# Optimization experiments

Measured on AMD Instinct MI355X. Metric: run time of the kernel, lower is better.

Reference implementation:

```python
import jax, jax.numpy as jnp
import numpy as np

B, C, L = 4, 256, 4096
H = 8
DK = C // H


def setup_inputs() -> dict:
    key = jax.random.key(0)
    kx, kq, kk, kv, kl = jax.random.split(key, 5)
    scale = 1.0 / np.sqrt(C)
    return {
        "x": jax.random.normal(kx, (B, C, L), dtype=jnp.float32),
        "Wq": jax.random.normal(kq, (C, C), dtype=jnp.float32) * scale,
        "Wk": jax.random.normal(kk, (C, C), dtype=jnp.float32) * scale,
        "Wv": jax.random.normal(kv, (C, C), dtype=jnp.float32) * scale,
        "Wl": jax.random.normal(kl, (C, C), dtype=jnp.float32) * scale,
    }


def reference(x, Wq, Wk, Wv, Wl):
    # Conv1d with kernel_size=1, no bias == channel-mixing matmul per position.
    def proj(W, t):  # W: [C_out, C_in], t: [B, C_in, L] -> [B, L, H, DK]
        y = jnp.einsum('oc,bcl->blo', W, t)
        return y.reshape(B, L, H, DK)

    q = proj(Wq, x)  # [B, L, H, DK]
    k = proj(Wk, x)
    v = proj(Wv, x)

    # scores: [B, H, L, L]
    scores = jnp.einsum('bqhd,bkhd->bhqk', q, k) / jnp.sqrt(jnp.float32(DK))
    p_attn = jax.nn.softmax(scores, axis=-1)
    # attention output with post-ReLU: [B, L, H, DK] -> [B, L, C]
    out = jax.nn.relu(jnp.einsum('bhqk,bkhd->bqhd', p_attn, v)).reshape(B, L, C)
    # last_conv: [B, C_out, L]
    return jnp.einsum('oc,blc->bol', Wl, out)
```

## Files before the change

kernel.cpp:

```cpp
#include <hip/hip_runtime.h>

#define L_DIM 4096
#define C_DIM 256
#define B_DIM 4
#define NH 8
#define DK 32

#define QSCALE 0.25507694f

typedef __bf16 bf16x8 __attribute__((ext_vector_type(8)));
typedef float  f32x4  __attribute__((ext_vector_type(4)));
typedef float  f32x16 __attribute__((ext_vector_type(16)));

static __device__ __forceinline__ unsigned pk_bf16(float lo, float hi) {
    unsigned a = __builtin_bit_cast(unsigned, lo) + 0x8000u;
    unsigned b = __builtin_bit_cast(unsigned, hi) + 0x8000u;
    return __builtin_amdgcn_perm(b, a, 0x07060302u);
}

__global__ __launch_bounds__(256) void transpose_x_kernel(
    const float* __restrict__ x, __bf16* __restrict__ xt)
{
    const int t  = threadIdx.x;
    const int l0 = blockIdx.x * 64;
    const int c0 = blockIdx.y * 64;
    const int b  = blockIdx.z;

    __shared__ __attribute__((aligned(16))) float T[64][65];

    {
        const int r  = t >> 2;
        const int lc = (t & 3) * 16;
        const float* xp = x + ((size_t)b * C_DIM + c0 + r) * L_DIM + l0 + lc;
        #pragma unroll
        for (int k = 0; k < 4; ++k)
            *(f32x4*)&T[r][lc + k * 4] = *(const f32x4*)(xp + k * 4);
    }
    __syncthreads();
    {
        const int l  = t >> 2;
        const int cc = (t & 3) * 16;
        unsigned u[8];
        #pragma unroll
        for (int i = 0; i < 8; ++i)
            u[i] = pk_bf16(T[cc + 2 * i][l], T[cc + 2 * i + 1][l]);
        __bf16* op = xt + ((size_t)b * L_DIM + l0 + l) * C_DIM + c0 + cc;
        *(uint4*)op       = make_uint4(u[0], u[1], u[2], u[3]);
        *(uint4*)(op + 8) = make_uint4(u[4], u[5], u[6], u[7]);
    }
}

__global__ __launch_bounds__(256) void proj_mfma_kernel(
    const __bf16* __restrict__ xt, const float* __restrict__ Wq,
    const float* __restrict__ Wk, const float* __restrict__ Wv,
    __bf16* __restrict__ Qb, __bf16* __restrict__ Kb, __bf16* __restrict__ Vb)
{
    const int t    = threadIdx.x;
    const int wave = t >> 6;
    const int lane = t & 63;
    const int n32  = lane & 31;
    const int hl   = lane >> 5;
    const int l0   = blockIdx.x * 128;
    const int ob   = blockIdx.y & 1;
    const int p    = blockIdx.y >> 1;
    const int b    = blockIdx.z;
    const float* W = (p == 0) ? Wq : ((p == 1) ? Wk : Wv);
    const float sc = (p == 0) ? QSCALE : 1.0f;

    __shared__ __attribute__((aligned(16))) __bf16 Wt[128][72];
    __shared__ __attribute__((aligned(16))) __bf16 Xs[128][72];

    const int wo  = t >> 1, wcc = (t & 1) * 32;
    const int xl  = t >> 1, xcc = (t & 1) * 32;
    const float*  wg = W + (size_t)(ob * 128 + wo) * C_DIM + wcc;
    const __bf16* xg = xt + ((size_t)b * L_DIM + l0 + xl) * C_DIM + xcc;

    const int moff = (wave & 1) * 64;
    const int noff = (wave >> 1) * 64;

    f32x16 acc[2][2];
    #pragma unroll
    for (int i = 0; i < 2; ++i)
        #pragma unroll
        for (int j = 0; j < 2; ++j)
            #pragma unroll
            for (int r = 0; r < 16; ++r) acc[i][j][r] = 0.f;

    unsigned wpk[16];
    bf16x8   xpr[4];
    #pragma unroll
    for (int k = 0; k < 8; ++k) {
        f32x4 wv = *(const f32x4*)(wg + k * 4);
        wpk[k * 2]     = pk_bf16(wv[0] * sc, wv[1] * sc);
        wpk[k * 2 + 1] = pk_bf16(wv[2] * sc, wv[3] * sc);
    }
    #pragma unroll
    for (int g = 0; g < 4; ++g) xpr[g] = *(const bf16x8*)(xg + g * 8);

    for (int bk = 0; bk < 4; ++bk) {
        __syncthreads();
        #pragma unroll
        for (int g = 0; g < 4; ++g) {
            *(uint4*)&Wt[wo][wcc + g * 8] =
                make_uint4(wpk[g*4], wpk[g*4+1], wpk[g*4+2], wpk[g*4+3]);
            *(bf16x8*)&Xs[xl][xcc + g * 8] = xpr[g];
        }
        if (bk < 3) {
            #pragma unroll
            for (int k = 0; k < 8; ++k) {
                f32x4 wv = *(const f32x4*)(wg + (bk + 1) * 64 + k * 4);
                wpk[k * 2]     = pk_bf16(wv[0] * sc, wv[1] * sc);
                wpk[k * 2 + 1] = pk_bf16(wv[2] * sc, wv[3] * sc);
            }
            #pragma unroll
            for (int g = 0; g < 4; ++g)
                xpr[g] = *(const bf16x8*)(xg + (bk + 1) * 64 + g * 8);
        }
        __syncthreads();

        #pragma unroll
        for (int ks = 0; ks < 4; ++ks) {
            bf16x8 a0 = *(const bf16x8*)&Wt[moff + n32     ][ks * 16 + hl * 8];
            bf16x8 a1 = *(const bf16x8*)&Wt[moff + 32 + n32][ks * 16 + hl * 8];
            bf16x8 b0 = *(const bf16x8*)&Xs[noff + n32     ][ks * 16 + hl * 8];
            bf16x8 b1 = *(const bf16x8*)&Xs[noff + 32 + n32][ks * 16 + hl * 8];
            acc[0][0] = __builtin_amdgcn_mfma_f32_32x32x16_bf16(a0, b0, acc[0][0], 0, 0, 0);
            acc[0][1] = __builtin_amdgcn_mfma_f32_32x32x16_bf16(a0, b1, acc[0][1], 0, 0, 0);
            acc[1][0] = __builtin_amdgcn_mfma_f32_32x32x16_bf16(a1, b0, acc[1][0], 0, 0, 0);
            acc[1][1] = __builtin_amdgcn_mfma_f32_32x32x16_bf16(a1, b1, acc[1][1], 0, 0, 0);
        }
    }

    #pragma unroll
    for (int mt = 0; mt < 2; ++mt) {
        const int o32 = ob * 128 + moff + mt * 32;
        const int h   = o32 >> 5;
        const int bh  = b * NH + h;
        #pragma unroll
        for (int nt = 0; nt < 2; ++nt) {
            const int l = l0 + noff + nt * 32 + n32;
            if (p < 2) {
                __bf16* out = ((p == 0) ? Qb : Kb) + ((size_t)bh * L_DIM + l) * DK;
                #pragma unroll
                for (int g = 0; g < 4; ++g) {
                    unsigned u0 = pk_bf16(acc[mt][nt][g*4],     acc[mt][nt][g*4+1]);
                    unsigned u1 = pk_bf16(acc[mt][nt][g*4+2],   acc[mt][nt][g*4+3]);
                    *(uint2*)(out + 4 * hl + 8 * g) = make_uint2(u0, u1);
                }
            } else {
                #pragma unroll
                for (int r = 0; r < 16; ++r) {
                    const int dk = (r & 3) + 4 * hl + 8 * (r >> 2);
                    Vb[((size_t)bh * DK + dk) * L_DIM + l] = (__bf16)acc[mt][nt][r];
                }
            }
        }
    }
}

__global__ __launch_bounds__(256) void attn_kernel(
    const __bf16* __restrict__ Q, const __bf16* __restrict__ K,
    const __bf16* __restrict__ V, __bf16* __restrict__ Op0,
    __bf16* __restrict__ Op1, float* __restrict__ Ls)
{
    const int tid   = threadIdx.x;
    const int wave  = tid >> 6;
    const int lane  = tid & 63;
    const int n32   = lane & 31;
    const int hl    = lane >> 5;
    const int h     = blockIdx.y;
    const int b     = blockIdx.z >> 1;
    const int khalf = blockIdx.z & 1;
    const int bh    = b * NH + h;
    const int q0    = blockIdx.x * 256 + wave * 64;
    const int kt0   = khalf * 32;

    __shared__ __attribute__((aligned(16))) __bf16 Ks[64][40];
    __shared__ __attribute__((aligned(16))) __bf16 Vs[32][72];

    bf16x8 qf[2][2];
    #pragma unroll
    for (int qt = 0; qt < 2; ++qt) {
        const __bf16* qp = Q + ((size_t)bh * L_DIM + q0 + qt * 32 + n32) * DK;
        qf[qt][0] = *(const bf16x8*)(qp + hl * 8);
        qf[qt][1] = *(const bf16x8*)(qp + 16 + hl * 8);
    }

    f32x16 oacc[2], lacc[2];
    #pragma unroll
    for (int qt = 0; qt < 2; ++qt)
        #pragma unroll
        for (int r = 0; r < 16; ++r) { oacc[qt][r] = 0.f; lacc[qt][r] = 0.f; }

    const f32x16 z16 = {};

    bf16x8 ones;
    #pragma unroll
    for (int j = 0; j < 8; ++j) ones[j] = (__bf16)1.0f;

    const __bf16* kg = K + (size_t)bh * L_DIM * DK + (tid >> 2) * DK + (tid & 3) * 8;
    const __bf16* vg = V + ((size_t)bh * DK + (tid >> 3)) * L_DIM + (tid & 7) * 8;
    __bf16* ksd = &Ks[tid >> 2][(tid & 3) * 8];
    const int va  = tid & 7;
    __bf16* vsd0 = &Vs[tid >> 3][(va >> 1) * 16 + (va & 1) * 4];
    __bf16* vsd1 = vsd0 + 8;

    bf16x8 kreg = *(const bf16x8*)(kg + (size_t)kt0 * 64 * DK);
    bf16x8 vreg = *(const bf16x8*)(vg + kt0 * 64);

    for (int kt = 0; kt < 32; ++kt) {
        __syncthreads();
        *(bf16x8*)ksd = kreg;
        union { bf16x8 v; uint2 u2[2]; } vv; vv.v = vreg;
        *(uint2*)vsd0 = vv.u2[0];
        *(uint2*)vsd1 = vv.u2[1];
        {
            const int nkt = kt0 + ((kt + 1) & 31);
            kreg = *(const bf16x8*)(kg + (size_t)nkt * 64 * DK);
            vreg = *(const bf16x8*)(vg + nkt * 64);
        }
        __syncthreads();

        bf16x8 kf[2][2];
        kf[0][0] = *(const bf16x8*)&Ks[n32     ][hl * 8];
        kf[0][1] = *(const bf16x8*)&Ks[n32     ][16 + hl * 8];
        kf[1][0] = *(const bf16x8*)&Ks[32 + n32][hl * 8];
        kf[1][1] = *(const bf16x8*)&Ks[32 + n32][16 + hl * 8];
        bf16x8 vf[4];
        vf[0] = *(const bf16x8*)&Vs[n32][     hl * 8];
        vf[1] = *(const bf16x8*)&Vs[n32][16 + hl * 8];
        vf[2] = *(const bf16x8*)&Vs[n32][32 + hl * 8];
        vf[3] = *(const bf16x8*)&Vs[n32][48 + hl * 8];

        #pragma unroll
        for (int mt = 0; mt < 2; ++mt) {
            #pragma unroll
            for (int qt = 0; qt < 2; ++qt) {
                f32x16 s = __builtin_amdgcn_mfma_f32_32x32x16_bf16(
                    kf[mt][0], qf[qt][0], z16, 0, 0, 0);
                s = __builtin_amdgcn_mfma_f32_32x32x16_bf16(
                    kf[mt][1], qf[qt][1], s, 0, 0, 0);

                float e[16];
                #pragma unroll
                for (int r = 0; r < 16; ++r) e[r] = __builtin_amdgcn_exp2f(s[r]);
                union { unsigned u[4]; bf16x8 v; } p0, p1;
                #pragma unroll
                for (int i = 0; i < 4; ++i) {
                    p0.u[i] = pk_bf16(e[2 * i],     e[2 * i + 1]);
                    p1.u[i] = pk_bf16(e[8 + 2 * i], e[8 + 2 * i + 1]);
                }

                oacc[qt] = __builtin_amdgcn_mfma_f32_32x32x16_bf16(
                    vf[mt * 2],     p0.v, oacc[qt], 0, 0, 0);
                lacc[qt] = __builtin_amdgcn_mfma_f32_32x32x16_bf16(
                    ones,           p0.v, lacc[qt], 0, 0, 0);
                oacc[qt] = __builtin_amdgcn_mfma_f32_32x32x16_bf16(
                    vf[mt * 2 + 1], p1.v, oacc[qt], 0, 0, 0);
                lacc[qt] = __builtin_amdgcn_mfma_f32_32x32x16_bf16(
                    ones,           p1.v, lacc[qt], 0, 0, 0);
            }
        }
    }

    __bf16* Op = khalf ? Op1 : Op0;
    #pragma unroll
    for (int qt = 0; qt < 2; ++qt) {
        const int l = q0 + qt * 32 + n32;
        __bf16* ap = Op + ((size_t)b * L_DIM + l) * C_DIM + h * 32 + 4 * hl;
        #pragma unroll
        for (int g = 0; g < 4; ++g) {
            *(uint2*)(ap + 8 * g) = make_uint2(
                pk_bf16(oacc[qt][g*4],     oacc[qt][g*4+1]),
                pk_bf16(oacc[qt][g*4+2],   oacc[qt][g*4+3]));
        }
        Ls[((size_t)khalf * B_DIM * NH + bh) * L_DIM + l] = lacc[qt][0];
    }
}

__global__ __launch_bounds__(256) void final_mfma_kernel(
    const __bf16* __restrict__ Op0, const __bf16* __restrict__ Op1,
    const float* __restrict__ Ls, const float* __restrict__ Wl,
    float* __restrict__ y)
{
    const int t    = threadIdx.x;
    const int wave = t >> 6;
    const int lane = t & 63;
    const int n32  = lane & 31;
    const int hl   = lane >> 5;
    const int l0   = blockIdx.x * 64;
    const int ob   = blockIdx.y;
    const int b    = blockIdx.z;

    __shared__ __attribute__((aligned(16))) __bf16 Wt[128][72];
    __shared__ __attribute__((aligned(16))) __bf16 Xs[64][72];

    const int wo  = t >> 1, wcc = (t & 1) * 32;
    const int xl  = t >> 2, xcc = (t & 3) * 16;
    const float* wg = Wl + (size_t)(ob * 128 + wo) * C_DIM + wcc;
    const size_t obase = ((size_t)b * L_DIM + l0 + xl) * C_DIM + xcc;

    float inv[4];
    {
        const int lidx = l0 + xl;
        #pragma unroll
        for (int bk = 0; bk < 4; ++bk) {
            const int hh = (bk * 64 + xcc) >> 5;
            const float l1 = Ls[((size_t)0 * B_DIM * NH + b * NH + hh) * L_DIM + lidx];
            const float l2 = Ls[((size_t)1 * B_DIM * NH + b * NH + hh) * L_DIM + lidx];
            inv[bk] = __builtin_amdgcn_rcpf(l1 + l2);
        }
    }

    const int moff = (wave & 1) * 64;
    const int noff = (wave >> 1) * 32;

    f32x16 acc[2];
    #pragma unroll
    for (int i = 0; i < 2; ++i)
        #pragma unroll
        for (int r = 0; r < 16; ++r) acc[i][r] = 0.f;

    unsigned wpk[16];
    bf16x8   o1r, o2r;
    #pragma unroll
    for (int k = 0; k < 8; ++k) {
        f32x4 wv = *(const f32x4*)(wg + k * 4);
        wpk[k * 2]     = pk_bf16(wv[0], wv[1]);
        wpk[k * 2 + 1] = pk_bf16(wv[2], wv[3]);
    }
    o1r = *(const bf16x8*)(Op0 + obase);
    o2r = *(const bf16x8*)(Op1 + obase);
    bf16x8 o1r2 = *(const bf16x8*)(Op0 + obase + 8);
    bf16x8 o2r2 = *(const bf16x8*)(Op1 + obase + 8);

    for (int bk = 0; bk < 4; ++bk) {
        __syncthreads();
        #pragma unroll
        for (int g = 0; g < 4; ++g)
            *(uint4*)&Wt[wo][wcc + g * 8] =
                make_uint4(wpk[g*4], wpk[g*4+1], wpk[g*4+2], wpk[g*4+3]);
        {
            unsigned u[4];
            #pragma unroll
            for (int i = 0; i < 4; ++i) {
                float v0 = ((float)o1r[2*i]   + (float)o2r[2*i]  ) * inv[bk];
                float v1 = ((float)o1r[2*i+1] + (float)o2r[2*i+1]) * inv[bk];
                v0 = v0 > 0.f ? v0 : 0.f;
                v1 = v1 > 0.f ? v1 : 0.f;
                u[i] = pk_bf16(v0, v1);
            }
            *(uint4*)&Xs[xl][xcc] = make_uint4(u[0], u[1], u[2], u[3]);
            #pragma unroll
            for (int i = 0; i < 4; ++i) {
                float v0 = ((float)o1r2[2*i]   + (float)o2r2[2*i]  ) * inv[bk];
                float v1 = ((float)o1r2[2*i+1] + (float)o2r2[2*i+1]) * inv[bk];
                v0 = v0 > 0.f ? v0 : 0.f;
                v1 = v1 > 0.f ? v1 : 0.f;
                u[i] = pk_bf16(v0, v1);
            }
            *(uint4*)&Xs[xl][xcc + 8] = make_uint4(u[0], u[1], u[2], u[3]);
        }
        if (bk < 3) {
            #pragma unroll
            for (int k = 0; k < 8; ++k) {
                f32x4 wv = *(const f32x4*)(wg + (bk + 1) * 64 + k * 4);
                wpk[k * 2]     = pk_bf16(wv[0], wv[1]);
                wpk[k * 2 + 1] = pk_bf16(wv[2], wv[3]);
            }
            o1r  = *(const bf16x8*)(Op0 + obase + (bk + 1) * 64);
            o2r  = *(const bf16x8*)(Op1 + obase + (bk + 1) * 64);
            o1r2 = *(const bf16x8*)(Op0 + obase + (bk + 1) * 64 + 8);
            o2r2 = *(const bf16x8*)(Op1 + obase + (bk + 1) * 64 + 8);
        }
        __syncthreads();

        #pragma unroll
        for (int ks = 0; ks < 4; ++ks) {
            bf16x8 a0 = *(const bf16x8*)&Wt[moff + n32     ][ks * 16 + hl * 8];
            bf16x8 a1 = *(const bf16x8*)&Wt[moff + 32 + n32][ks * 16 + hl * 8];
            bf16x8 b0 = *(const bf16x8*)&Xs[noff + n32     ][ks * 16 + hl * 8];
            acc[0] = __builtin_amdgcn_mfma_f32_32x32x16_bf16(a0, b0, acc[0], 0, 0, 0);
            acc[1] = __builtin_amdgcn_mfma_f32_32x32x16_bf16(a1, b0, acc[1], 0, 0, 0);
        }
    }

    #pragma unroll
    for (int mt = 0; mt < 2; ++mt) {
        #pragma unroll
        for (int r = 0; r < 16; ++r) {
            const int o = ob * 128 + moff + mt * 32 + (r & 3) + 4 * hl + 8 * (r >> 2);
            y[((size_t)b * C_DIM + o) * L_DIM + l0 + noff + n32] = acc[mt][r];
        }
    }
}

extern "C" void kernel_launch(void* const* d_in, const int* in_sizes, int n_in,
                              void* d_out, int out_size, void* d_ws, size_t ws_size,
                              hipStream_t stream)
{
    const float* x  = (const float*)d_in[0];
    const float* Wq = (const float*)d_in[1];
    const float* Wk = (const float*)d_in[2];
    const float* Wv = (const float*)d_in[3];
    const float* Wl = (const float*)d_in[4];
    float* y = (float*)d_out;

    const size_t n = (size_t)B_DIM * NH * L_DIM * DK;
    __bf16* Qb  = (__bf16*)d_ws;
    __bf16* Kb  = Qb + n;
    __bf16* Vb  = Kb + n;
    __bf16* Xt  = Vb + n;
    __bf16* Op0 = Xt;
    __bf16* Op1 = Xt + n;
    float*  Ls  = (float*)(Op1 + n);

    transpose_x_kernel<<<dim3(L_DIM/64, C_DIM/64, B_DIM), 256, 0, stream>>>(x, Xt);
    proj_mfma_kernel<<<dim3(L_DIM/128, 6, B_DIM), 256, 0, stream>>>(
        Xt, Wq, Wk, Wv, Qb, Kb, Vb);
    attn_kernel<<<dim3(L_DIM/256, NH, B_DIM * 2), 256, 0, stream>>>(
        Qb, Kb, Vb, Op0, Op1, Ls);
    final_mfma_kernel<<<dim3(L_DIM/64, 2, B_DIM), 256, 0, stream>>>(
        Op0, Op1, Ls, Wl, y);
}
```

Baseline: 217.1 us.

## Double-buffer K/V tiles in LDS and use native bf16 vector conversion

The attention inner loop now ping-pongs between two LDS buffers for K and V. This removes one of the two barriers per iteration, and the next tile's shared-memory store overlaps with the MFMA work on the current tile. The manual round-bias bf16 packing is replaced with __builtin_convertvector, which may map to the hardware's packed bf16 conversion but changes rounding to round-to-nearest-even. LDS usage doubles, and the loop is unrolled by 2.

```diff
diff --git a/kernel.cpp b/kernel.cpp
--- a/kernel.cpp
+++ b/kernel.cpp
@@ -10,6 +10,7 @@
 
 typedef __bf16 bf16x8 __attribute__((ext_vector_type(8)));
 typedef float  f32x4  __attribute__((ext_vector_type(4)));
+typedef float  f32x8  __attribute__((ext_vector_type(8)));
 typedef float  f32x16 __attribute__((ext_vector_type(16)));
 
 static __device__ __forceinline__ unsigned pk_bf16(float lo, float hi) {
@@ -175,8 +176,8 @@
     const int q0    = blockIdx.x * 256 + wave * 64;
     const int kt0   = khalf * 32;
 
-    __shared__ __attribute__((aligned(16))) __bf16 Ks[64][40];
-    __shared__ __attribute__((aligned(16))) __bf16 Vs[32][72];
+    __shared__ __attribute__((aligned(16))) __bf16 Ks[2][64][40];
+    __shared__ __attribute__((aligned(16))) __bf16 Vs[2][32][72];
 
     bf16x8 qf[2][2];
     #pragma unroll
@@ -200,37 +201,46 @@
 
     const __bf16* kg = K + (size_t)bh * L_DIM * DK + (tid >> 2) * DK + (tid & 3) * 8;
     const __bf16* vg = V + ((size_t)bh * DK + (tid >> 3)) * L_DIM + (tid & 7) * 8;
-    __bf16* ksd = &Ks[tid >> 2][(tid & 3) * 8];
-    const int va  = tid & 7;
-    __bf16* vsd0 = &Vs[tid >> 3][(va >> 1) * 16 + (va & 1) * 4];
-    __bf16* vsd1 = vsd0 + 8;
+    const int kr = tid >> 2, kc = (tid & 3) * 8;
+    const int va = tid & 7;
+    const int vr = tid >> 3, vc = (va >> 1) * 16 + (va & 1) * 4;
 
     bf16x8 kreg = *(const bf16x8*)(kg + (size_t)kt0 * 64 * DK);
     bf16x8 vreg = *(const bf16x8*)(vg + kt0 * 64);
-
+    *(bf16x8*)&Ks[0][kr][kc] = kreg;
+    {
+        union { bf16x8 v; uint2 u2[2]; } vv; vv.v = vreg;
+        *(uint2*)&Vs[0][vr][vc]     = vv.u2[0];
+        *(uint2*)&Vs[0][vr][vc + 8] = vv.u2[1];
+    }
+    kreg = *(const bf16x8*)(kg + (size_t)(kt0 + 1) * 64 * DK);
+    vreg = *(const bf16x8*)(vg + (kt0 + 1) * 64);
+
+    #pragma unroll 2
     for (int kt = 0; kt < 32; ++kt) {
+        const int cur = kt & 1;
         __syncthreads();
-        *(bf16x8*)ksd = kreg;
-        union { bf16x8 v; uint2 u2[2]; } vv; vv.v = vreg;
-        *(uint2*)vsd0 = vv.u2[0];
-        *(uint2*)vsd1 = vv.u2[1];
-        {
-            const int nkt = kt0 + ((kt + 1) & 31);
+
+        bf16x8 kf[2][2];
+        kf[0][0] = *(const bf16x8*)&Ks[cur][n32     ][hl * 8];
+        kf[0][1] = *(const bf16x8*)&Ks[cur][n32     ][16 + hl * 8];
+        kf[1][0] = *(const bf16x8*)&Ks[cur][32 + n32][hl * 8];
+        kf[1][1] = *(const bf16x8*)&Ks[cur][32 + n32][16 + hl * 8];
+        bf16x8 vf[4];
+        vf[0] = *(const bf16x8*)&Vs[cur][n32][     hl * 8];
+        vf[1] = *(const bf16x8*)&Vs[cur][n32][16 + hl * 8];
+        vf[2] = *(const bf16x8*)&Vs[cur][n32][32 + hl * 8];
+        vf[3] = *(const bf16x8*)&Vs[cur][n32][48 + hl * 8];
+
+        if (kt < 31) {
+            *(bf16x8*)&Ks[cur ^ 1][kr][kc] = kreg;
+            union { bf16x8 v; uint2 u2[2]; } vv; vv.v = vreg;
+            *(uint2*)&Vs[cur ^ 1][vr][vc]     = vv.u2[0];
+            *(uint2*)&Vs[cur ^ 1][vr][vc + 8] = vv.u2[1];
+            const int nkt = kt0 + ((kt + 2) & 31);
             kreg = *(const bf16x8*)(kg + (size_t)nkt * 64 * DK);
             vreg = *(const bf16x8*)(vg + nkt * 64);
         }
-        __syncthreads();
-
-        bf16x8 kf[2][2];
-        kf[0][0] = *(const bf16x8*)&Ks[n32     ][hl * 8];
-        kf[0][1] = *(const bf16x8*)&Ks[n32     ][16 + hl * 8];
-        kf[1][0] = *(const bf16x8*)&Ks[32 + n32][hl * 8];
-        kf[1][1] = *(const bf16x8*)&Ks[32 + n32][16 + hl * 8];
-        bf16x8 vf[4];
-        vf[0] = *(const bf16x8*)&Vs[n32][     hl * 8];
-        vf[1] = *(const bf16x8*)&Vs[n32][16 + hl * 8];
-        vf[2] = *(const bf16x8*)&Vs[n32][32 + hl * 8];
-        vf[3] = *(const bf16x8*)&Vs[n32][48 + hl * 8];
 
         #pragma unroll
         for (int mt = 0; mt < 2; ++mt) {
@@ -241,24 +251,23 @@
                 s = __builtin_amdgcn_mfma_f32_32x32x16_bf16(
                     kf[mt][1], qf[qt][1], s, 0, 0, 0);
 
-                float e[16];
+                f32x8 e0, e1;
                 #pragma unroll
-                for (int r = 0; r < 16; ++r) e[r] = __builtin_amdgcn_exp2f(s[r]);
-                union { unsigned u[4]; bf16x8 v; } p0, p1;
-                #pragma unroll
-                for (int i = 0; i < 4; ++i) {
-                    p0.u[i] = pk_bf16(e[2 * i],     e[2 * i + 1]);
-                    p1.u[i] = pk_bf16(e[8 + 2 * i], e[8 + 2 * i + 1]);
+                for (int r = 0; r < 8; ++r) {
+                    e0[r] = __builtin_amdgcn_exp2f(s[r]);
+                    e1[r] = __builtin_amdgcn_exp2f(s[8 + r]);
                 }
+                bf16x8 p0 = __builtin_convertvector(e0, bf16x8);
+                bf16x8 p1 = __builtin_convertvector(e1, bf16x8);
 
                 oacc[qt] = __builtin_amdgcn_mfma_f32_32x32x16_bf16(
-                    vf[mt * 2],     p0.v, oacc[qt], 0, 0, 0);
+                    vf[mt * 2],     p0, oacc[qt], 0, 0, 0);
                 lacc[qt] = __builtin_amdgcn_mfma_f32_32x32x16_bf16(
-                    ones,           p0.v, lacc[qt], 0, 0, 0);
+                    ones,           p0, lacc[qt], 0, 0, 0);
                 oacc[qt] = __builtin_amdgcn_mfma_f32_32x32x16_bf16(
-                    vf[mt * 2 + 1], p1.v, oacc[qt], 0, 0, 0);
+                    vf[mt * 2 + 1], p1, oacc[qt], 0, 0, 0);
                 lacc[qt] = __builtin_amdgcn_mfma_f32_32x32x16_bf16(
-                    ones,           p1.v, lacc[qt], 0, 0, 0);
+                    ones,           p1, lacc[qt], 0, 0, 0);
             }
         }
     }
```

Measured after the change: 211.2 us. -2.8%, faster.

## Make attention single-wave blocks loading K/V directly from global memory

Applied to the files above, without the earlier changes.

Reshapes the attention kernel from 256-thread blocks that stage K and V tiles through shared memory behind two barriers into 64-thread single-wave blocks. Each wave now reads its K and V MFMA fragments straight from global memory, which it expects to hit in L2, and the grid is four times larger. This removes LDS traffic and __syncthreads stalls, but K/V global reads are now repeated per wave and there is no explicit register prefetch, so load latency must be hidden by occupancy. The manual bf16 packing of the exponentials is also replaced with __builtin_convertvector, which may map to a native packed convert and changes rounding to round-to-nearest-even.

```diff
diff --git a/kernel.cpp b/kernel.cpp
--- a/kernel.cpp
+++ b/kernel.cpp
@@ -10,6 +10,7 @@
 
 typedef __bf16 bf16x8 __attribute__((ext_vector_type(8)));
 typedef float  f32x4  __attribute__((ext_vector_type(4)));
+typedef float  f32x8  __attribute__((ext_vector_type(8)));
 typedef float  f32x16 __attribute__((ext_vector_type(16)));
 
 static __device__ __forceinline__ unsigned pk_bf16(float lo, float hi) {
@@ -158,25 +159,19 @@
     }
 }
 
-__global__ __launch_bounds__(256) void attn_kernel(
+__global__ __launch_bounds__(64, 4) void attn_kernel(
     const __bf16* __restrict__ Q, const __bf16* __restrict__ K,
     const __bf16* __restrict__ V, __bf16* __restrict__ Op0,
     __bf16* __restrict__ Op1, float* __restrict__ Ls)
 {
     const int tid   = threadIdx.x;
-    const int wave  = tid >> 6;
-    const int lane  = tid & 63;
-    const int n32   = lane & 31;
-    const int hl    = lane >> 5;
+    const int n32   = tid & 31;
+    const int hl    = tid >> 5;
     const int h     = blockIdx.y;
     const int b     = blockIdx.z >> 1;
     const int khalf = blockIdx.z & 1;
     const int bh    = b * NH + h;
-    const int q0    = blockIdx.x * 256 + wave * 64;
-    const int kt0   = khalf * 32;
-
-    __shared__ __attribute__((aligned(16))) __bf16 Ks[64][40];
-    __shared__ __attribute__((aligned(16))) __bf16 Vs[32][72];
+    const int q0    = blockIdx.x * 64;
 
     bf16x8 qf[2][2];
     #pragma unroll
@@ -198,67 +193,45 @@
     #pragma unroll
     for (int j = 0; j < 8; ++j) ones[j] = (__bf16)1.0f;
 
-    const __bf16* kg = K + (size_t)bh * L_DIM * DK + (tid >> 2) * DK + (tid & 3) * 8;
-    const __bf16* vg = V + ((size_t)bh * DK + (tid >> 3)) * L_DIM + (tid & 7) * 8;
-    __bf16* ksd = &Ks[tid >> 2][(tid & 3) * 8];
-    const int va  = tid & 7;
-    __bf16* vsd0 = &Vs[tid >> 3][(va >> 1) * 16 + (va & 1) * 4];
-    __bf16* vsd1 = vsd0 + 8;
-
-    bf16x8 kreg = *(const bf16x8*)(kg + (size_t)kt0 * 64 * DK);
-    bf16x8 vreg = *(const bf16x8*)(vg + kt0 * 64);
+    const __bf16* kp = K + ((size_t)bh * L_DIM + (size_t)khalf * 2048) * DK;
+    const __bf16* vp = V + ((size_t)bh * DK + n32) * L_DIM + khalf * 2048 + 4 * hl;
 
     for (int kt = 0; kt < 32; ++kt) {
-        __syncthreads();
-        *(bf16x8*)ksd = kreg;
-        union { bf16x8 v; uint2 u2[2]; } vv; vv.v = vreg;
-        *(uint2*)vsd0 = vv.u2[0];
-        *(uint2*)vsd1 = vv.u2[1];
-        {
-            const int nkt = kt0 + ((kt + 1) & 31);
-            kreg = *(const bf16x8*)(kg + (size_t)nkt * 64 * DK);
-            vreg = *(const bf16x8*)(vg + nkt * 64);
-        }
-        __syncthreads();
-
-        bf16x8 kf[2][2];
-        kf[0][0] = *(const bf16x8*)&Ks[n32     ][hl * 8];
-        kf[0][1] = *(const bf16x8*)&Ks[n32     ][16 + hl * 8];
-        kf[1][0] = *(const bf16x8*)&Ks[32 + n32][hl * 8];
-        kf[1][1] = *(const bf16x8*)&Ks[32 + n32][16 + hl * 8];
-        bf16x8 vf[4];
-        vf[0] = *(const bf16x8*)&Vs[n32][     hl * 8];
-        vf[1] = *(const bf16x8*)&Vs[n32][16 + hl * 8];
-        vf[2] = *(const bf16x8*)&Vs[n32][32 + hl * 8];
-        vf[3] = *(const bf16x8*)&Vs[n32][48 + hl * 8];
-
         #pragma unroll
         for (int mt = 0; mt < 2; ++mt) {
+            const __bf16* krow = kp + (size_t)(kt * 64 + mt * 32 + n32) * DK + hl * 8;
+            bf16x8 ka = *(const bf16x8*)krow;
+            bf16x8 kb = *(const bf16x8*)(krow + 16);
+            const __bf16* vrow = vp + kt * 64 + mt * 32;
+            union { uint2 u2[2]; bf16x8 v; } va_, vb_;
+            va_.u2[0] = *(const uint2*)(vrow);
+            va_.u2[1] = *(const uint2*)(vrow + 8);
+            vb_.u2[0] = *(const uint2*)(vrow + 16);
+            vb_.u2[1] = *(const uint2*)(vrow + 24);
+
             #pragma unroll
             for (int qt = 0; qt < 2; ++qt) {
                 f32x16 s = __builtin_amdgcn_mfma_f32_32x32x16_bf16(
-                    kf[mt][0], qf[qt][0], z16, 0, 0, 0);
+                    ka, qf[qt][0], z16, 0, 0, 0);
                 s = __builtin_amdgcn_mfma_f32_32x32x16_bf16(
-                    kf[mt][1], qf[qt][1], s, 0, 0, 0);
-
-                float e[16];
+                    kb, qf[qt][1], s, 0, 0, 0);
+
                 #pragma unroll
-                for (int r = 0; r < 16; ++r) e[r] = __builtin_amdgcn_exp2f(s[r]);
-                union { unsigned u[4]; bf16x8 v; } p0, p1;
+                for (int r = 0; r < 16; ++r) s[r] = __builtin_amdgcn_exp2f(s[r]);
+                f32x8 e0, e1;
                 #pragma unroll
-                for (int i = 0; i < 4; ++i) {
-                    p0.u[i] = pk_bf16(e[2 * i],     e[2 * i + 1]);
-                    p1.u[i] = pk_bf16(e[8 + 2 * i], e[8 + 2 * i + 1]);
-                }
+                for (int r = 0; r < 8; ++r) { e0[r] = s[r]; e1[r] = s[8 + r]; }
+                bf16x8 p0 = __builtin_convertvector(e0, bf16x8);
+                bf16x8 p1 = __builtin_convertvector(e1, bf16x8);
 
                 oacc[qt] = __builtin_amdgcn_mfma_f32_32x32x16_bf16(
-                    vf[mt * 2],     p0.v, oacc[qt], 0, 0, 0);
+                    va_.v, p0, oacc[qt], 0, 0, 0);
                 lacc[qt] = __builtin_amdgcn_mfma_f32_32x32x16_bf16(
-                    ones,           p0.v, lacc[qt], 0, 0, 0);
+                    ones,  p0, lacc[qt], 0, 0, 0);
                 oacc[qt] = __builtin_amdgcn_mfma_f32_32x32x16_bf16(
-                    vf[mt * 2 + 1], p1.v, oacc[qt], 0, 0, 0);
+                    vb_.v, p1, oacc[qt], 0, 0, 0);
                 lacc[qt] = __builtin_amdgcn_mfma_f32_32x32x16_bf16(
-                    ones,           p1.v, lacc[qt], 0, 0, 0);
+                    ones,  p1, lacc[qt], 0, 0, 0);
             }
         }
     }
@@ -418,7 +391,7 @@
     transpose_x_kernel<<<dim3(L_DIM/64, C_DIM/64, B_DIM), 256, 0, stream>>>(x, Xt);
     proj_mfma_kernel<<<dim3(L_DIM/128, 6, B_DIM), 256, 0, stream>>>(
         Xt, Wq, Wk, Wv, Qb, Kb, Vb);
-    attn_kernel<<<dim3(L_DIM/256, NH, B_DIM * 2), 256, 0, stream>>>(
+    attn_kernel<<<dim3(L_DIM/64, NH, B_DIM * 2), 64, 0, stream>>>(
         Qb, Kb, Vb, Op0, Op1, Ls);
     final_mfma_kernel<<<dim3(L_DIM/64, 2, B_DIM), 256, 0, stream>>>(
         Op0, Op1, Ls, Wl, y);
```

After: 260.7 us. 20.0% more time.
